# Performance work log

Measured on AMD Instinct MI355X. Metric: run time of the kernel, lower is better.

Reference implementation:

```python
import jax, jax.numpy as jnp
import numpy as np


def setup_inputs() -> dict:
    key = jax.random.key(0)
    k_w, k_xi, k_u = jax.random.split(key, 3)
    N, d, M, L, B = 4096, 512, 256, 16, 1024
    W = 2 * L + 1  # window width = 33
    # xavier-normal-ish scale for weight (fan_in=d, fan_out=M*W per torch xavier on last dim pairs)
    w_scale = (2.0 / (W + d)) ** 0.5
    xi_scale = (2.0 / (M + N + 2 * L)) ** 0.5
    weight = jax.random.normal(k_w, (M, W, d), dtype=jnp.float32) * w_scale
    bias = jnp.zeros((M, W, 1), dtype=jnp.float32)
    xi = jax.random.normal(k_xi, (M, N + 2 * L), dtype=jnp.float32) * xi_scale
    u = jax.random.normal(k_u, (B, d), dtype=jnp.float32)
    return {"u": u, "weight": weight, "bias": bias, "xi": xi}


def reference(u, weight, bias, xi):
    # weight: [M, W, d], bias: [M, W, 1], xi: [M, N + W - 1], u: [B, d]
    M, W, d = weight.shape
    N = xi.shape[1] - (W - 1)
    # first_step: G[m, j, b] = sigmoid(sum_k weight[m,j,k] * u[b,k] + bias[m,j])
    G = jax.nn.sigmoid(jnp.einsum('mjd,bd->mjb', weight, u) + bias)  # [M, W, B]
    # im2col-style unfold of xi into overlapping windows, replacing the N-step Python loop
    idx = jnp.arange(N)[:, None] + jnp.arange(W)[None, :]  # [N, W]
    Xw = xi[:, idx]  # [M, N, W]
    # out[n, b] = sum_{m, j} xi[m, n+j] * G[m, j, b]  == torch.cat of iter_prod rows
    return jnp.einsum('mnj,mjb->nb', Xw, G)  # [N, B]
```

## Files before the change

### kernel.cpp

```cpp
#include <hip/hip_runtime.h>
#include <hip/hip_bf16.h>

typedef __attribute__((ext_vector_type(8))) short bf16x8;
typedef __attribute__((ext_vector_type(4))) float f32x4;
typedef unsigned int u32;
typedef unsigned short u16;

#define XI_ROW 4128
#define KP     8448
#define NB     1024
#define NN     4096
#define DDIM   512

__device__ __forceinline__ u16 f2bf(float f) {
  union { float f; unsigned u; } c; c.f = f;
  return (u16)((c.u + 0x7FFFu + ((c.u >> 16) & 1u)) >> 16);
}
__device__ __forceinline__ float bf2f(u16 h) {
  union { u32 u; float f; } c; c.u = ((u32)h) << 16; return c.f;
}
__device__ __forceinline__ u32 pk2bf(float a, float b) {
  return (u32)f2bf(a) | ((u32)f2bf(b) << 16);
}
__device__ __forceinline__ void gld16(const u16* g, u16* l) {
  __builtin_amdgcn_global_load_lds(
      (const __attribute__((address_space(1))) u32*)(const void*)g,
      (__attribute__((address_space(3))) u32*)(void*)l, 16, 0, 0);
}

#define BAR() __builtin_amdgcn_s_barrier()
#define LGKM0() asm volatile("s_waitcnt lgkmcnt(0)" ::: "memory")
#define LGKM8() asm volatile("s_waitcnt lgkmcnt(8)" ::: "memory")
#define WAITVM(N) asm volatile("s_waitcnt vmcnt(" #N ")" ::: "memory")
#define SCHED0() __builtin_amdgcn_sched_barrier(0)
#define MEMF() asm volatile("" ::: "memory")

__global__ __launch_bounds__(256) void k_prep(
    const float* __restrict__ w, const float* __restrict__ u,
    u16* __restrict__ Wbf, u16* __restrict__ Ubf) {
  const int bx = blockIdx.x, t = threadIdx.x;
  if (bx < 4224) {
    int kp = bx * 2 + (t >> 7), tl = t & 127;
    int m = kp & 255, j = kp >> 8;
    float4 v = ((const float4*)(w + (size_t)(m * 33 + j) * DDIM))[tl];
    ((uint2*)(Wbf + (size_t)kp * DDIM))[tl] =
        make_uint2(pk2bf(v.x, v.y), pk2bf(v.z, v.w));
  } else {
    int b = (bx - 4224) * 2 + (t >> 7), tl = t & 127;
    float4 v = ((const float4*)(u + (size_t)b * DDIM))[tl];
    ((uint2*)(Ubf + (size_t)b * DDIM))[tl] =
        make_uint2(pk2bf(v.x, v.y), pk2bf(v.z, v.w));
  }
}

template<int KSTEPS, int AS, int BS>
__device__ __forceinline__ void gemm_pipeline(
    const u16* __restrict__ aSrc, const u16* __restrict__ bSrc,
    u16* As0, u16* As1, u16* Bl0, u16* Bl1,
    int wid, int wr, int wc, int rl, int kg, int rl7,
    f32x4 (&acc)[4][4]) {

  auto stage = [&](u16* Ab, u16* Bb, int kk) {
#pragma unroll
    for (int i = 0; i < 4; ++i)
      gld16(aSrc + (size_t)i * 8 * AS + kk, &Ab[(wid * 4 + i) * 512]);
#pragma unroll
    for (int i = 0; i < 4; ++i)
      gld16(bSrc + (size_t)i * 8 * BS + kk, &Bb[(wid * 4 + i) * 512]);
  };
  auto compute = [&](const u16* Ab, const u16* Bb) {
#pragma unroll
    for (int kh = 0; kh < 2; ++kh) {
      bf16x8 af[4], bfv[4];
#pragma unroll
      for (int fm = 0; fm < 4; ++fm)
        af[fm] = *(const bf16x8*)&Ab[(wr * 64 + fm * 16 + rl) * 64 +
                                     (((kh * 4 + kg) ^ rl7) * 8)];
#pragma unroll
      for (int fn = 0; fn < 4; ++fn)
        bfv[fn] = *(const bf16x8*)&Bb[(wc * 64 + fn * 16 + rl) * 64 +
                                      (((kh * 4 + kg) ^ rl7) * 8)];
      __builtin_amdgcn_s_setprio(1);
#pragma unroll
      for (int fm = 0; fm < 4; ++fm)
#pragma unroll
        for (int fn = 0; fn < 4; ++fn)
          acc[fm][fn] = __builtin_amdgcn_mfma_f32_16x16x32_bf16(
              af[fm], bfv[fn], acc[fm][fn], 0, 0, 0);
      __builtin_amdgcn_s_setprio(0);
    }
  };

  stage(As0, Bl0, 0);
  WAITVM(0);
  BAR();
#pragma unroll 1
  for (int ts = 0; ts < KSTEPS - 2; ts += 2) {
    stage(As1, Bl1, (ts + 1) * 64);
    WAITVM(8);
    BAR();
    compute(As0, Bl0);
    BAR();
    stage(As0, Bl0, (ts + 2) * 64);
    WAITVM(8);
    BAR();
    compute(As1, Bl1);
    BAR();
  }
  stage(As1, Bl1, (KSTEPS - 1) * 64);
  WAITVM(8);
  BAR();
  compute(As0, Bl0);
  BAR();
  WAITVM(0);
  BAR();
  compute(As1, Bl1);
}

__global__ __launch_bounds__(256) void k_gemm1(
    const u16* __restrict__ Wbf, const u16* __restrict__ Ubf,
    const float* __restrict__ Bsrc, u16* __restrict__ Gt,
    const float* __restrict__ xi, u16* __restrict__ xiT) {
  __shared__ u16 lds1[32768];
  const int bx = blockIdx.x, t = threadIdx.x;

  if (bx >= 528) {
    u16 (*tile)[33] = (u16(*)[33])lds1;
    int id = bx - 528;
    int cblk = id % 129, mblk = id / 129;
    int c0 = cblk * 32, m0 = mblk * 32;
    int tx = t & 31, ty = t >> 5;
#pragma unroll
    for (int i = 0; i < 4; ++i)
      tile[ty + i * 8][tx] = f2bf(xi[(size_t)(m0 + ty + i * 8) * XI_ROW + c0 + tx]);
    __syncthreads();
#pragma unroll
    for (int i = 0; i < 4; ++i)
      xiT[(size_t)(c0 + ty + i * 8) * 256 + m0 + tx] = tile[tx][ty + i * 8];
    return;
  }

  u16* As0 = lds1;
  u16* As1 = lds1 + 8192;
  u16* Bl0 = lds1 + 16384;
  u16* Bl1 = lds1 + 24576;
  const int r0 = (bx % 66) * 128;
  const int b0 = (bx / 66) * 128;
  const int lane = t & 63, wid = t >> 6;
  const int wr = wid >> 1, wc = wid & 1;
  const int rl = lane & 15, kg = lane >> 4, rl7 = rl & 7;
  const int lr = lane >> 3, lc = (lane & 7) ^ (lr & 7);
  const u16* aSrc = Wbf + (size_t)(r0 + wid * 32 + lr) * DDIM + lc * 8;
  const u16* bSrc = Ubf + (size_t)(b0 + wid * 32 + lr) * DDIM + lc * 8;

  f32x4 acc[4][4] = {};
  gemm_pipeline<8, DDIM, DDIM>(aSrc, bSrc, As0, As1, Bl0, Bl1,
                               wid, wr, wc, rl, kg, rl7, acc);

  __syncthreads();
  u16* Lt = lds1;
#pragma unroll
  for (int fm = 0; fm < 4; ++fm) {
    int kloc = wr * 64 + fm * 16 + kg * 4;
    int kbase = r0 + kloc;
    float b4[4];
#pragma unroll
    for (int r = 0; r < 4; ++r) {
      int kk = kbase + r;
      b4[r] = Bsrc[(kk & 255) * 33 + (kk >> 8)];
    }
#pragma unroll
    for (int fn = 0; fn < 4; ++fn) {
      int bloc = wc * 64 + fn * 16 + rl;
      u16 o[4];
#pragma unroll
      for (int r = 0; r < 4; ++r) {
        float x = acc[fm][fn][r] + b4[r];
        o[r] = f2bf(1.0f / (1.0f + __expf(-x)));
      }
      *(uint2*)&Lt[bloc * 136 + kloc] =
          make_uint2((u32)o[0] | ((u32)o[1] << 16),
                     (u32)o[2] | ((u32)o[3] << 16));
    }
  }
  __syncthreads();
  const int bl = t >> 4, j = t & 15;
#pragma unroll
  for (int p = 0; p < 8; ++p) {
    int bloc = p * 16 + bl;
    uint4 v = *(const uint4*)&Lt[bloc * 136 + j * 8];
    *(uint4*)(Gt + (size_t)(b0 + bloc) * KP + r0 + j * 8) = v;
  }
}

__global__ __launch_bounds__(512, 2) void k_gemm2(
    const u16* __restrict__ xiT, const u16* __restrict__ Gt,
    float* __restrict__ Out, u16* __restrict__ Part, int allbf) {
  __shared__ u16 lds[65536];
  const int lid = blockIdx.x;
  const int b0 = (lid & 3) * 256;
  const int ks = (lid >> 2) & 3;
  const int n0 = (lid >> 4) * 256;
  const int kOff = (ks < 2) ? ks * 2176 : 4352 + (ks - 2) * 2048;
  const int nt = (ks < 2) ? 34 : 32;

  const int t = threadIdx.x, lane = t & 63, wid = t >> 6;
  const int wr = wid >> 2, wc = wid & 3;
  const int rl = lane & 15, kg = lane >> 4, rl7 = rl & 7;
  const int sr = lane >> 3;
  const int sc = (lane & 7) ^ sr;

  const u16* aS = xiT + (size_t)(n0 + wid * 16 + sr) * 256 + kOff + sc * 8;
  const u16* bS = Gt  + (size_t)(b0 + wid * 16 + sr) * KP  + kOff + sc * 8;

  f32x4 acc[8][4] = {};
  bf16x8 af[8], b01[4], b23[4];

  auto stA = [&](int tile, int half, int buf) {
    u16* d = lds + (buf * 4 + half) * 8192 + wid * 1024;
    const u16* s = aS + (size_t)half * 32768 + (size_t)tile * 64;
    gld16(s, d);
    gld16(s + 2048, d + 512);
  };
  auto stB = [&](int tile, int half, int buf) {
    u16* d = lds + (buf * 4 + 2 + half) * 8192 + wid * 1024;
    const u16* s = bS + (size_t)half * 128 * KP + (size_t)tile * 64;
    gld16(s, d);
    gld16(s + (size_t)8 * KP, d + 512);
  };
  auto rdA = [&](int buf, int sub) {
    const u16* p = lds + (buf * 4 + wr) * 8192;
#pragma unroll
    for (int q = 0; q < 4; ++q)
#pragma unroll
      for (int kh = 0; kh < 2; ++kh)
        af[q * 2 + kh] = *(const bf16x8*)
            &p[((sub * 4 + q) * 16 + rl) * 64 + (((kh * 4 + kg) ^ rl7) * 8)];
  };
  auto rdB = [&](int buf, int sub, bf16x8 (&bq)[4]) {
    const u16* p = lds + (buf * 4 + 2 + (wc >> 1)) * 8192;
#pragma unroll
    for (int q = 0; q < 2; ++q)
#pragma unroll
      for (int kh = 0; kh < 2; ++kh)
        bq[q * 2 + kh] = *(const bf16x8*)
            &p[((wc & 1) * 64 + (sub * 2 + q) * 16 + rl) * 64 +
               (((kh * 4 + kg) ^ rl7) * 8)];
  };
  auto mm = [&](int sm, int sn, bf16x8 (&bq)[4]) {
    __builtin_amdgcn_s_setprio(1);
#pragma unroll
    for (int q = 0; q < 4; ++q)
#pragma unroll
      for (int p = 0; p < 2; ++p)
#pragma unroll
        for (int kh = 0; kh < 2; ++kh)
          acc[sm * 4 + q][sn * 2 + p] = __builtin_amdgcn_mfma_f32_16x16x32_bf16(
              af[q * 2 + kh], bq[p * 2 + kh], acc[sm * 4 + q][sn * 2 + p], 0, 0, 0);
    __builtin_amdgcn_s_setprio(0);
  };

  auto runIter = [&](int T, bool s2, bool s3) {
    rdA(0, 0); stB(T + 1, 1, 1);
    LGKM8(); SCHED0(); BAR(); LGKM0(); SCHED0(); mm(0, 0, b01);
    rdB(0, 1, b23); stA(T + 1, 0, 1);
    SCHED0(); BAR(); LGKM0(); SCHED0(); mm(0, 1, b23);
    rdA(0, 1); stA(T + 1, 1, 1);
    SCHED0(); BAR(); LGKM0(); SCHED0(); mm(1, 0, b01);
    if (s2) { stB(T + 2, 0, 0); WAITVM(2); } else { WAITVM(0); }
    SCHED0(); BAR(); MEMF();
    rdB(1, 0, b01);
    SCHED0(); mm(1, 1, b23);
    rdA(1, 0); if (s2) stB(T + 2, 1, 0);
    LGKM8(); SCHED0(); BAR(); LGKM0(); SCHED0(); mm(0, 0, b01);
    rdB(1, 1, b23); if (s2) stA(T + 2, 0, 0);
    SCHED0(); BAR(); LGKM0(); SCHED0(); mm(0, 1, b23);
    rdA(1, 1); if (s2) stA(T + 2, 1, 0);
    SCHED0(); BAR(); LGKM0(); SCHED0(); mm(1, 0, b01);
    if (s3) { stB(T + 3, 0, 1); WAITVM(2); }
    else if (s2) { WAITVM(0); }
    SCHED0(); BAR(); MEMF();
    rdB(0, 0, b01);
    SCHED0(); mm(1, 1, b23);
  };

  stA(0, 0, 0); stA(0, 1, 0); stB(0, 0, 0); stB(0, 1, 0);
  stB(1, 0, 1);
  WAITVM(2);
  BAR();
  MEMF();
  rdB(0, 0, b01);

  const int nIter = nt >> 1;
#pragma unroll 1
  for (int it = 0; it < nIter - 1; ++it) runIter(it * 2, true, true);
  runIter((nIter - 1) * 2, false, false);

  if (!allbf && ks == 0) {
#pragma unroll
    for (int fm = 0; fm < 8; ++fm)
#pragma unroll
      for (int fn = 0; fn < 4; ++fn) {
        int n = n0 + wr * 128 + fm * 16 + kg * 4;
        int b = b0 + wc * 64 + fn * 16 + rl;
#pragma unroll
        for (int r = 0; r < 4; ++r)
          Out[(size_t)(n + r) * NB + b] = acc[fm][fn][r];
      }
  } else {
    int slot = allbf ? ks : (ks - 1);
    u16* P = Part + (size_t)slot * (NN * NB);
#pragma unroll
    for (int fm = 0; fm < 8; ++fm)
#pragma unroll
      for (int fn = 0; fn < 4; ++fn) {
        int n = n0 + wr * 128 + fm * 16 + kg * 4;
        int b = b0 + wc * 64 + fn * 16 + rl;
#pragma unroll
        for (int r = 0; r < 4; ++r)
          P[(size_t)(n + r) * NB + b] = f2bf(acc[fm][fn][r]);
      }
  }
}

__global__ __launch_bounds__(256) void k_reduce(float* __restrict__ Out,
                                                const u16* __restrict__ Part,
                                                int allbf) {
  size_t i8 = ((size_t)blockIdx.x * 256 + threadIdx.x) * 8;
  float a[8];
  int np;
  if (allbf) {
#pragma unroll
    for (int q = 0; q < 8; ++q) a[q] = 0.f;
    np = 4;
  } else {
    float4 x = *(const float4*)(Out + i8);
    float4 y = *(const float4*)(Out + i8 + 4);
    a[0] = x.x; a[1] = x.y; a[2] = x.z; a[3] = x.w;
    a[4] = y.x; a[5] = y.y; a[6] = y.z; a[7] = y.w;
    np = 3;
  }
  for (int p = 0; p < np; ++p) {
    uint4 v = *(const uint4*)(Part + (size_t)p * (NN * NB) + i8);
    a[0] += bf2f((u16)(v.x & 0xFFFFu)); a[1] += bf2f((u16)(v.x >> 16));
    a[2] += bf2f((u16)(v.y & 0xFFFFu)); a[3] += bf2f((u16)(v.y >> 16));
    a[4] += bf2f((u16)(v.z & 0xFFFFu)); a[5] += bf2f((u16)(v.z >> 16));
    a[6] += bf2f((u16)(v.w & 0xFFFFu)); a[7] += bf2f((u16)(v.w >> 16));
  }
  *(float4*)(Out + i8)     = make_float4(a[0], a[1], a[2], a[3]);
  *(float4*)(Out + i8 + 4) = make_float4(a[4], a[5], a[6], a[7]);
}

extern "C" void kernel_launch(void* const* d_in, const int* in_sizes, int n_in,
                              void* d_out, int out_size, void* d_ws, size_t ws_size,
                              hipStream_t stream) {
  const float* u  = (const float*)d_in[0];
  const float* w  = (const float*)d_in[1];
  const float* bs = (const float*)d_in[2];
  const float* xi = (const float*)d_in[3];
  float* out = (float*)d_out;

  u16* xiT  = (u16*)d_ws;
  u16* Gt   = (u16*)((char*)d_ws + 2113536);
  u16* Wbf  = (u16*)((char*)d_ws + 19415040);
  u16* Ubf  = (u16*)((char*)d_ws + 28065792);
  u16* Part = (u16*)((char*)d_ws + 19415040);
  const int allbf = (ws_size >= 52969472ull) ? 1 : 0;

  k_prep<<<4736, 256, 0, stream>>>(w, u, Wbf, Ubf);
  k_gemm1<<<1560, 256, 0, stream>>>(Wbf, Ubf, bs, Gt, xi, xiT);
  k_gemm2<<<256, 512, 0, stream>>>(xiT, Gt, out, Part, allbf);
  k_reduce<<<2048, 256, 0, stream>>>(out, Part, allbf);
}
```

Measured before the change: 99.92 us.

## Shrink gemm2 tiles to 256x128 with 32-wide K steps and more blocks

Reworks the second GEMM kernel to use a 256x128 output tile per block with K-tiles of 32 instead of 64, cutting LDS from 128 KB to 48 KB and raising the launch-bounds occupancy hint. The grid doubles to 512 blocks, and the K-split becomes four equal chunks of 2112. The pipeline becomes a simpler double buffer with a full vmcnt wait each half-iteration. The goal is better CU coverage and latency hiding. The cost is lower arithmetic intensity per block, more global traffic for the shared operand, and less overlap of loads inside each block.

```diff
diff --git a/kernel.cpp b/kernel.cpp
--- a/kernel.cpp
+++ b/kernel.cpp
@@ -30,10 +30,8 @@
 
 #define BAR() __builtin_amdgcn_s_barrier()
 #define LGKM0() asm volatile("s_waitcnt lgkmcnt(0)" ::: "memory")
-#define LGKM8() asm volatile("s_waitcnt lgkmcnt(8)" ::: "memory")
 #define WAITVM(N) asm volatile("s_waitcnt vmcnt(" #N ")" ::: "memory")
 #define SCHED0() __builtin_amdgcn_sched_barrier(0)
-#define MEMF() asm volatile("" ::: "memory")
 
 __global__ __launch_bounds__(256) void k_prep(
     const float* __restrict__ w, const float* __restrict__ u,
@@ -193,115 +191,100 @@
   }
 }
 
-__global__ __launch_bounds__(512, 2) void k_gemm2(
+__global__ __launch_bounds__(512, 4) void k_gemm2(
     const u16* __restrict__ xiT, const u16* __restrict__ Gt,
     float* __restrict__ Out, u16* __restrict__ Part, int allbf) {
-  __shared__ u16 lds[65536];
+  __shared__ u16 lds[24576];
   const int lid = blockIdx.x;
-  const int b0 = (lid & 3) * 256;
-  const int ks = (lid >> 2) & 3;
-  const int n0 = (lid >> 4) * 256;
-  const int kOff = (ks < 2) ? ks * 2176 : 4352 + (ks - 2) * 2048;
-  const int nt = (ks < 2) ? 34 : 32;
+  const int b0 = (lid & 7) * 128;
+  const int ks = (lid >> 3) & 3;
+  const int n0 = (lid >> 5) * 256;
+  const int kOff = ks * 2112;
 
   const int t = threadIdx.x, lane = t & 63, wid = t >> 6;
-  const int wr = wid >> 2, wc = wid & 3;
-  const int rl = lane & 15, kg = lane >> 4, rl7 = rl & 7;
-  const int sr = lane >> 3;
-  const int sc = (lane & 7) ^ sr;
-
-  const u16* aS = xiT + (size_t)(n0 + wid * 16 + sr) * 256 + kOff + sc * 8;
-  const u16* bS = Gt  + (size_t)(b0 + wid * 16 + sr) * KP  + kOff + sc * 8;
-
-  f32x4 acc[8][4] = {};
-  bf16x8 af[8], b01[4], b23[4];
-
-  auto stA = [&](int tile, int half, int buf) {
-    u16* d = lds + (buf * 4 + half) * 8192 + wid * 1024;
-    const u16* s = aS + (size_t)half * 32768 + (size_t)tile * 64;
-    gld16(s, d);
-    gld16(s + 2048, d + 512);
-  };
-  auto stB = [&](int tile, int half, int buf) {
-    u16* d = lds + (buf * 4 + 2 + half) * 8192 + wid * 1024;
-    const u16* s = bS + (size_t)half * 128 * KP + (size_t)tile * 64;
-    gld16(s, d);
-    gld16(s + (size_t)8 * KP, d + 512);
-  };
-  auto rdA = [&](int buf, int sub) {
-    const u16* p = lds + (buf * 4 + wr) * 8192;
-#pragma unroll
-    for (int q = 0; q < 4; ++q)
-#pragma unroll
-      for (int kh = 0; kh < 2; ++kh)
-        af[q * 2 + kh] = *(const bf16x8*)
-            &p[((sub * 4 + q) * 16 + rl) * 64 + (((kh * 4 + kg) ^ rl7) * 8)];
-  };
-  auto rdB = [&](int buf, int sub, bf16x8 (&bq)[4]) {
-    const u16* p = lds + (buf * 4 + 2 + (wc >> 1)) * 8192;
-#pragma unroll
-    for (int q = 0; q < 2; ++q)
-#pragma unroll
-      for (int kh = 0; kh < 2; ++kh)
-        bq[q * 2 + kh] = *(const bf16x8*)
-            &p[((wc & 1) * 64 + (sub * 2 + q) * 16 + rl) * 64 +
-               (((kh * 4 + kg) ^ rl7) * 8)];
-  };
-  auto mm = [&](int sm, int sn, bf16x8 (&bq)[4]) {
+  const int wr = wid >> 1, wc = wid & 1;
+  const int rl = lane & 15, kg = lane >> 4;
+  const int sq = lane >> 2;
+  const int swsrc = (lane & 3) ^ ((lane >> 3) & 3);
+  const int rsw = (rl >> 1) & 3;
+
+  const u16* aS = xiT + (size_t)(n0 + wid * 32 + sq) * 256 + kOff + swsrc * 8;
+  const u16* bS = Gt  + (size_t)(b0 + wid * 16 + sq) * KP  + kOff + swsrc * 8;
+
+  u16* A0 = lds;
+  u16* A1 = lds + 8192;
+  u16* B0 = lds + 16384;
+  u16* B1 = lds + 20480;
+
+  f32x4 acc[4][4] = {};
+  bf16x8 af[4], bfv[4];
+
+  auto stA = [&](int tile, int i, u16* Ab) {
+    gld16(aS + (size_t)i * 16 * 256 + (size_t)tile * 32,
+          Ab + (wid * 32 + i * 16) * 32);
+  };
+  auto stB = [&](int tile, u16* Bb) {
+    gld16(bS + (size_t)tile * 32, Bb + wid * 512);
+  };
+  auto rdA = [&](const u16* Ab, int fm) {
+    af[fm] = *(const bf16x8*)&Ab[(wr * 64 + fm * 16 + rl) * 32 +
+                                 ((kg ^ rsw) << 3)];
+  };
+  auto rdB = [&](const u16* Bb, int fn) {
+    bfv[fn] = *(const bf16x8*)&Bb[(wc * 64 + fn * 16 + rl) * 32 +
+                                  ((kg ^ rsw) << 3)];
+  };
+  auto mm = [&](int sm, int sn) {
     __builtin_amdgcn_s_setprio(1);
 #pragma unroll
-    for (int q = 0; q < 4; ++q)
-#pragma unroll
-      for (int p = 0; p < 2; ++p)
-#pragma unroll
-        for (int kh = 0; kh < 2; ++kh)
-          acc[sm * 4 + q][sn * 2 + p] = __builtin_amdgcn_mfma_f32_16x16x32_bf16(
-              af[q * 2 + kh], bq[p * 2 + kh], acc[sm * 4 + q][sn * 2 + p], 0, 0, 0);
+    for (int i = 0; i < 2; ++i)
+#pragma unroll
+      for (int j = 0; j < 2; ++j)
+        acc[sm * 2 + i][sn * 2 + j] = __builtin_amdgcn_mfma_f32_16x16x32_bf16(
+            af[sm * 2 + i], bfv[sn * 2 + j], acc[sm * 2 + i][sn * 2 + j],
+            0, 0, 0);
     __builtin_amdgcn_s_setprio(0);
   };
 
-  auto runIter = [&](int T, bool s2, bool s3) {
-    rdA(0, 0); stB(T + 1, 1, 1);
-    LGKM8(); SCHED0(); BAR(); LGKM0(); SCHED0(); mm(0, 0, b01);
-    rdB(0, 1, b23); stA(T + 1, 0, 1);
-    SCHED0(); BAR(); LGKM0(); SCHED0(); mm(0, 1, b23);
-    rdA(0, 1); stA(T + 1, 1, 1);
-    SCHED0(); BAR(); LGKM0(); SCHED0(); mm(1, 0, b01);
-    if (s2) { stB(T + 2, 0, 0); WAITVM(2); } else { WAITVM(0); }
-    SCHED0(); BAR(); MEMF();
-    rdB(1, 0, b01);
-    SCHED0(); mm(1, 1, b23);
-    rdA(1, 0); if (s2) stB(T + 2, 1, 0);
-    LGKM8(); SCHED0(); BAR(); LGKM0(); SCHED0(); mm(0, 0, b01);
-    rdB(1, 1, b23); if (s2) stA(T + 2, 0, 0);
-    SCHED0(); BAR(); LGKM0(); SCHED0(); mm(0, 1, b23);
-    rdA(1, 1); if (s2) stA(T + 2, 1, 0);
-    SCHED0(); BAR(); LGKM0(); SCHED0(); mm(1, 0, b01);
-    if (s3) { stB(T + 3, 0, 1); WAITVM(2); }
-    else if (s2) { WAITVM(0); }
-    SCHED0(); BAR(); MEMF();
-    rdB(0, 0, b01);
-    SCHED0(); mm(1, 1, b23);
-  };
-
-  stA(0, 0, 0); stA(0, 1, 0); stB(0, 0, 0); stB(0, 1, 0);
-  stB(1, 0, 1);
-  WAITVM(2);
-  BAR();
-  MEMF();
-  rdB(0, 0, b01);
-
-  const int nIter = nt >> 1;
+  auto runIter = [&](int T, bool s2) {
+    rdA(A0, 0); rdA(A0, 1); rdB(B0, 0); rdB(B0, 1);
+    stA(T + 1, 0, A1);
+    SCHED0(); BAR(); LGKM0(); SCHED0(); mm(0, 0);
+    rdB(B0, 2); rdB(B0, 3);
+    stA(T + 1, 1, A1);
+    SCHED0(); BAR(); LGKM0(); SCHED0(); mm(0, 1);
+    rdA(A0, 2); rdA(A0, 3);
+    stB(T + 1, B1);
+    SCHED0(); BAR(); LGKM0(); SCHED0(); mm(1, 0);
+    WAITVM(0);
+    SCHED0(); BAR(); SCHED0(); mm(1, 1);
+    rdA(A1, 0); rdA(A1, 1); rdB(B1, 0); rdB(B1, 1);
+    if (s2) stA(T + 2, 0, A0);
+    SCHED0(); BAR(); LGKM0(); SCHED0(); mm(0, 0);
+    rdB(B1, 2); rdB(B1, 3);
+    if (s2) stA(T + 2, 1, A0);
+    SCHED0(); BAR(); LGKM0(); SCHED0(); mm(0, 1);
+    rdA(A1, 2); rdA(A1, 3);
+    if (s2) stB(T + 2, B0);
+    SCHED0(); BAR(); LGKM0(); SCHED0(); mm(1, 0);
+    WAITVM(0);
+    SCHED0(); BAR(); SCHED0(); mm(1, 1);
+  };
+
+  stA(0, 0, A0); stA(0, 1, A0); stB(0, B0);
+  WAITVM(0);
+  BAR();
+
 #pragma unroll 1
-  for (int it = 0; it < nIter - 1; ++it) runIter(it * 2, true, true);
-  runIter((nIter - 1) * 2, false, false);
+  for (int it = 0; it < 32; ++it) runIter(it * 2, true);
+  runIter(64, false);
 
   if (!allbf && ks == 0) {
 #pragma unroll
-    for (int fm = 0; fm < 8; ++fm)
+    for (int fm = 0; fm < 4; ++fm)
 #pragma unroll
       for (int fn = 0; fn < 4; ++fn) {
-        int n = n0 + wr * 128 + fm * 16 + kg * 4;
+        int n = n0 + wr * 64 + fm * 16 + kg * 4;
         int b = b0 + wc * 64 + fn * 16 + rl;
 #pragma unroll
         for (int r = 0; r < 4; ++r)
@@ -311,10 +294,10 @@
     int slot = allbf ? ks : (ks - 1);
     u16* P = Part + (size_t)slot * (NN * NB);
 #pragma unroll
-    for (int fm = 0; fm < 8; ++fm)
+    for (int fm = 0; fm < 4; ++fm)
 #pragma unroll
       for (int fn = 0; fn < 4; ++fn) {
-        int n = n0 + wr * 128 + fm * 16 + kg * 4;
+        int n = n0 + wr * 64 + fm * 16 + kg * 4;
         int b = b0 + wc * 64 + fn * 16 + rl;
 #pragma unroll
         for (int r = 0; r < 4; ++r)
@@ -369,6 +352,6 @@
 
   k_prep<<<4736, 256, 0, stream>>>(w, u, Wbf, Ubf);
   k_gemm1<<<1560, 256, 0, stream>>>(Wbf, Ubf, bs, Gt, xi, xiT);
-  k_gemm2<<<256, 512, 0, stream>>>(xiT, Gt, out, Part, allbf);
+  k_gemm2<<<512, 512, 0, stream>>>(xiT, Gt, out, Part, allbf);
   k_reduce<<<2048, 256, 0, stream>>>(out, Part, allbf);
 }
```

Result: slower. 113.2 us (+13.3%).
